# Performance work log

Hardware: AMD Instinct MI355X
Metric: run time of the kernel (lower is better)

## Reference

```python
import jax, jax.numpy as jnp
import numpy as np

D_MODEL = 1024
N_HEADS = 16
POINT_DIM = 4
PLUCKER_DIM = 6
PAIRS4 = [(0, 1), (0, 2), (0, 3), (1, 2), (1, 3), (2, 3)]
_J6 = jnp.array([[0, 0, 0, 0, 0, 1], [0, 0, 0, 0, -1, 0], [0, 0, 0, 1, 0, 0],
                 [0, 0, 1, 0, 0, 0], [0, -1, 0, 0, 0, 0], [1, 0, 0, 0, 0, 0]], dtype=jnp.float32)


def exterior(p1, p2):
    # p1, p2: [..., point_dim] -> normalized Plucker coords [..., 6]
    L = jnp.stack([p1[..., i] * p2[..., j] - p1[..., j] * p2[..., i] for i, j in PAIRS4], axis=-1)
    n = jnp.linalg.norm(L, axis=-1, keepdims=True)
    return L / jnp.maximum(n, 1e-12)


def setup_inputs() -> dict:
    key = jax.random.key(0)
    ks = jax.random.split(key, 16)
    B, T, D, H, pd = 2, 1024, D_MODEL, N_HEADS, POINT_DIM
    s = 0.02
    return {
        "x": jax.random.normal(ks[0], (B, T, D), dtype=jnp.float32),
        "qkv_w": jax.random.normal(ks[1], (D, 3 * D), dtype=jnp.float32) * s,
        "qkv_b": jnp.zeros((3 * D,), dtype=jnp.float32),
        "w1_write_w": jax.random.normal(ks[2], (2 * D, pd * H), dtype=jnp.float32) * s,
        "w2_write_w": jax.random.normal(ks[3], (D, pd * H), dtype=jnp.float32) * s,
        "w1_read_w": jax.random.normal(ks[4], (D, pd * H), dtype=jnp.float32) * s,
        "w2_read_w": jax.random.normal(ks[5], (D, pd * H), dtype=jnp.float32) * s,
        "mem_value_w": jax.random.normal(ks[6], (D, D), dtype=jnp.float32) * s,
        "mem_value_b": jnp.zeros((D,), dtype=jnp.float32),
        "mem_gate_w": jax.random.normal(ks[7], (D, H), dtype=jnp.float32) * s,
        "mem_gate_b": jnp.zeros((H,), dtype=jnp.float32),
        "mem_scale": jnp.full((H,), 0.1, dtype=jnp.float32),
        "out_w": jax.random.normal(ks[8], (D, D), dtype=jnp.float32) * s,
        "out_b": jnp.zeros((D,), dtype=jnp.float32),
        "decay_logits": jnp.full((H,), 4.6, dtype=jnp.float32),
        "J": _J6,
    }


def reference(x, qkv_w, qkv_b, w1_write_w, w2_write_w, w1_read_w, w2_read_w,
              mem_value_w, mem_value_b, mem_gate_w, mem_gate_b, mem_scale,
              out_w, out_b, decay_logits, J):
    B, T, D = x.shape
    H = N_HEADS
    dh = D // H
    pd = POINT_DIM
    scale = dh ** (-0.5)

    # ---- standard causal attention ----
    qkv = (x @ qkv_w + qkv_b).reshape(B, T, 3, H, dh)
    q = jnp.transpose(qkv[:, :, 0], (0, 2, 1, 3))  # [B,H,T,dh]
    k = jnp.transpose(qkv[:, :, 1], (0, 2, 1, 3))
    v = jnp.transpose(qkv[:, :, 2], (0, 2, 1, 3))
    scores = jnp.einsum('bhtd,bhsd->bhts', q, k) * scale
    causal_mask = jnp.triu(jnp.ones((T, T), dtype=bool), k=1)
    scores = jnp.where(causal_mask, -jnp.inf, scores)
    attn = jax.nn.softmax(scores, axis=-1)
    seq_out = jnp.einsum('bhts,bhsd->bthd', attn, v).reshape(B, T, D)

    # ---- trigram write lines ----
    z = jnp.zeros((B, 1, D), dtype=x.dtype)
    x_prev1 = jnp.concatenate([z, x[:, :-1]], axis=1)
    x_prev2 = jnp.concatenate([z, z, x[:, :-2]], axis=1)
    trigram_ctx = jnp.concatenate([x_prev2, x_prev1], axis=-1)  # [B,T,2D]
    w1 = (trigram_ctx @ w1_write_w).reshape(B, T, H, pd)
    w2 = (x @ w2_write_w).reshape(B, T, H, pd)
    write_lines = exterior(w1, w2)  # [B,T,H,6]
    r1 = (x @ w1_read_w).reshape(B, T, H, pd)
    r2 = (x @ w2_read_w).reshape(B, T, H, pd)
    read_lines = exterior(r1, r2)  # [B,T,H,6]

    # ---- Plucker incidence + decay weighting ----
    J_write = jnp.einsum('bshi,ij->bshj', write_lines, J)
    incidence = jnp.einsum('bthi,bshi->bhts', read_lines, J_write)  # [B,H,T,T]
    incidence_sq = incidence ** 2
    positions = jnp.arange(T, dtype=x.dtype)
    diffs = positions[:, None] - positions[None, :]  # [T,T]
    decays = jax.nn.sigmoid(decay_logits)  # [H]
    # strictly-causal (diffs>0) decay weights; masked_fill(triu diag=0, 0) == (diffs>0)
    weights = jnp.where(diffs[None] > 0, decays[:, None, None] ** jnp.maximum(diffs, 0.0)[None], 0.0)
    mem_score = jnp.sum(incidence_sq * weights[None], axis=-1)  # [B,H,T]

    # ---- gated memory value ----
    mem_val = x @ mem_value_w + mem_value_b  # [B,T,D]
    gate = jax.nn.sigmoid(x @ mem_gate_w + mem_gate_b)  # [B,T,H]
    mem_score_t = jnp.transpose(mem_score, (0, 2, 1))  # [B,T,H]
    gated = jax.nn.sigmoid(mem_score_t * mem_scale[None, None, :]) * gate
    gated = jnp.mean(gated, axis=-1, keepdims=True)  # [B,T,1]

    return (seq_out + gated * mem_val) @ out_w + out_b
```

## Files before the change

### kernel.cpp

```cpp
#include <hip/hip_runtime.h>
#include <hip/hip_bf16.h>
#include <stdint.h>


typedef __attribute__((ext_vector_type(8))) __bf16 bf16v8;
typedef __attribute__((ext_vector_type(8))) short  s16x8;
typedef __attribute__((ext_vector_type(4))) float  f32x4;

#define LOG2E 1.4426950408889634f

__device__ __forceinline__ float bf2f(short s) {
  union { uint32_t u; float f; } cv; cv.u = ((uint32_t)(uint16_t)s) << 16; return cv.f;
}
__device__ __forceinline__ short f2bf(float f) {
  union { float f; uint32_t u; } cv; cv.f = f;
  uint32_t r = cv.u + 0x7fffu + ((cv.u >> 16) & 1u);
  return (short)(r >> 16);
}

__device__ __forceinline__ f32x4 mfma_bf16(s16x8 a, s16x8 b, f32x4 c) {
  return __builtin_amdgcn_mfma_f32_16x16x32_bf16(
      __builtin_bit_cast(bf16v8, a), __builtin_bit_cast(bf16v8, b), c, 0, 0, 0);
}

__device__ __forceinline__ void gload_lds16(const void* g, void* l) {
  __builtin_amdgcn_global_load_lds(
      (const __attribute__((address_space(1))) uint32_t*)g,
      (__attribute__((address_space(3))) uint32_t*)l, 16, 0, 0);
}


__global__ __launch_bounds__(256) void k_prep(
    const float* __restrict__ x, const float* __restrict__ qkvw,
    const float* __restrict__ mvw, const float* __restrict__ ow,
    const float* __restrict__ w1w, const float* __restrict__ w2w,
    const float* __restrict__ r1w, const float* __restrict__ r2w,
    const float* __restrict__ gw, const float* __restrict__ qkvb,
    const float* __restrict__ mvb,
    short* __restrict__ xb, short* __restrict__ btall, short* __restrict__ owT,
    float* __restrict__ biasAll) {
  __shared__ float tile[32][33];
  const int bid = blockIdx.x;
  const int tid = threadIdx.x;
  if (bid < 2048) {
    const int i = (bid * 256 + tid) * 4;
    float4 v = *(const float4*)&x[i];
    short4 o;
    o.x = f2bf(v.x); o.y = f2bf(v.y); o.z = f2bf(v.z); o.w = f2bf(v.w);
    *(short4*)&xb[i] = o;
    return;
  }
  if (bid < 7168) {
    const float* W; short* Wt; int N, u;
    if (bid < 5120)      { W = qkvw; Wt = btall;                       N = 3072; u = bid - 2048; }
    else if (bid < 6144) { W = mvw;  Wt = btall + (size_t)3072 * 1024; N = 1024; u = bid - 5120; }
    else                 { W = ow;   Wt = owT;                         N = 1024; u = bid - 6144; }
    const int ntiles = N >> 5;
    const int n0 = (u % ntiles) * 32, k0 = (u / ntiles) * 32;
    const int tx = tid & 31, ty = tid >> 5;
#pragma unroll
    for (int i = 0; i < 4; i++)
      tile[ty + i * 8][tx] = W[(size_t)(k0 + ty + i * 8) * N + n0 + tx];
    __syncthreads();
#pragma unroll
    for (int i = 0; i < 4; i++)
      Wt[(size_t)(n0 + ty + i * 8) * 1024 + k0 + tx] = f2bf(tile[tx][ty + i * 8]);
    return;
  }
  if (bid < 8704) {
    const int idx = (bid - 7168) * 256 + tid;
    const int r = idx >> 10, k = idx & 1023;
    float v = 0.f;
    if (r < 64)       v = w1w[(size_t)k * 64 + r];
    else if (r < 128) v = w1w[(size_t)(1024 + k) * 64 + (r - 64)];
    else if (r < 192) v = w2w[(size_t)k * 64 + (r - 128)];
    else if (r < 256) v = r1w[(size_t)k * 64 + (r - 192)];
    else if (r < 320) v = r2w[(size_t)k * 64 + (r - 256)];
    else if (r < 336) v = gw[(size_t)k * 16 + (r - 320)];
    btall[(size_t)4096 * 1024 + idx] = f2bf(v);
    return;
  }
  {
    const int i = (bid - 8704) * 256 + tid;
    if (i < 4480) {
      float v = 0.f;
      if (i < 3072) v = qkvb[i];
      else if (i < 4096) v = mvb[i - 3072];
      biasAll[i] = v;
    }
  }
}


__global__ __launch_bounds__(256) void k_gemmF(const short* __restrict__ A,
                                               const short* __restrict__ Bt,
                                               short* __restrict__ C,
                                               const float* __restrict__ bias,
                                               float* __restrict__ projf,
                                               short* __restrict__ vtg) {
  const int N = 4480, K = 1024;
  __shared__ short pool[32768];
  short* Asp = pool;
  short* Bsp = pool + 16384;
  const int m0 = blockIdx.x * 128, n0 = blockIdx.y * 128;
  const int tid = threadIdx.x;
  const int lane = tid & 63, w = tid >> 6;
  const int wr = (w >> 1) * 64, wc = (w & 1) * 64;
  const int l15 = lane & 15, lg = lane >> 4;
  const int r0e = tid >> 2, c0e = (tid & 3) << 3;
  const int r1e = (tid + 256) >> 2, c1e = ((tid + 256) & 3) << 3;
  f32x4 acc[4][4] = {};

  auto stage = [&](int buf, int k0) {
    gload_lds16(A + (size_t)(m0 + r0e) * K + k0 + c0e, Asp + buf * 4096 + tid * 8);
    gload_lds16(A + (size_t)(m0 + r1e) * K + k0 + c1e, Asp + buf * 4096 + (tid + 256) * 8);
    gload_lds16(Bt + (size_t)(n0 + r0e) * K + k0 + c0e, Bsp + buf * 4096 + tid * 8);
    gload_lds16(Bt + (size_t)(n0 + r1e) * K + k0 + c1e, Bsp + buf * 4096 + (tid + 256) * 8);
  };

  stage(0, 0);
  stage(1, 32);
  __syncthreads();

  const int nkt = K >> 5;
  for (int kp = 0; kp < nkt; kp += 2) {
    if (kp + 2 < nkt) stage((kp + 2) & 3, (kp + 2) << 5);
    if (kp + 3 < nkt) stage((kp + 3) & 3, (kp + 3) << 5);
#pragma unroll
    for (int u = 0; u < 2; u++) {
      const int cur = (kp + u) & 3;
      s16x8 af[4], bfv[4];
#pragma unroll
      for (int i = 0; i < 4; i++) {
        af[i]  = *(const s16x8*)&Asp[cur * 4096 + (wr + i * 16 + l15) * 32 + lg * 8];
        bfv[i] = *(const s16x8*)&Bsp[cur * 4096 + (wc + i * 16 + l15) * 32 + lg * 8];
      }
      __builtin_amdgcn_s_setprio(1);
#pragma unroll
      for (int mi = 0; mi < 4; mi++)
#pragma unroll
        for (int ni = 0; ni < 4; ni++)
          acc[mi][ni] = mfma_bf16(af[mi], bfv[ni], acc[mi][ni]);
      __builtin_amdgcn_s_setprio(0);
    }
    __syncthreads();
  }

  const bool isproj = (n0 >= 4096);
  const bool isv = (n0 >= 2048) && (n0 < 3072);
  if (isv) {
    short* T = pool;
#pragma unroll
    for (int mi = 0; mi < 4; mi++)
#pragma unroll
      for (int ni = 0; ni < 4; ni++) {
        const int colLoc = wc + ni * 16 + l15;
        const float bv = bias[n0 + colLoc];
#pragma unroll
        for (int r = 0; r < 4; r++)
          T[colLoc * 136 + wr + mi * 16 + lg * 4 + r] = f2bf(acc[mi][ni][r] + bv);
      }
    __syncthreads();
    const int b = m0 >> 10, t0 = m0 & 1023;
#pragma unroll
    for (int q = 0; q < 8; q++) {
      const int colLoc = w * 32 + q * 4 + (lane >> 4);
      const int chunk = lane & 15;
      s16x8 v = *(const s16x8*)&T[colLoc * 136 + chunk * 8];
      const int cd = n0 + colLoc - 2048;
      const int hh = cd >> 6, d = cd & 63;
      *(s16x8*)&vtg[((size_t)((b << 4) + hh) * 64 + d) * 1024 + t0 + chunk * 8] = v;
    }
    return;
  }
#pragma unroll
  for (int mi = 0; mi < 4; mi++)
#pragma unroll
    for (int ni = 0; ni < 4; ni++) {
      const int col = n0 + wc + ni * 16 + l15;
      const float bv = bias[col];
#pragma unroll
      for (int r = 0; r < 4; r++) {
        const int row = m0 + wr + mi * 16 + lg * 4 + r;
        const float v = acc[mi][ni][r] + bv;
        if (isproj) projf[(size_t)row * 384 + (col - 4096)] = v;
        else        C[(size_t)row * 4480 + col] = f2bf(v);
      }
    }
}


template <int BM>
__global__ __launch_bounds__(256) void k_gemm(const short* __restrict__ A,
                                              const short* __restrict__ Bt,
                                              float* __restrict__ C,
                                              const float* __restrict__ bias,
                                              int N, int K) {
  constexpr int MI = BM / 32;
  __shared__ short As[4][BM * 32];
  __shared__ short Bs[4][128 * 32];
  const int m0 = blockIdx.x * BM, n0 = blockIdx.y * 128;
  const int tid = threadIdx.x;
  const int lane = tid & 63, w = tid >> 6;
  const int wr = (w >> 1) * (BM / 2), wc = (w & 1) * 64;
  const int l15 = lane & 15, lg = lane >> 4;
  const int r0e = tid >> 2, c0e = (tid & 3) << 3;
  const int r1e = (tid + 256) >> 2, c1e = ((tid + 256) & 3) << 3;
  f32x4 acc[MI][4] = {};

  auto stage = [&](int buf, int k0) {
    if constexpr (BM == 128) {
      gload_lds16(A + (size_t)(m0 + r0e) * K + k0 + c0e, &As[buf][tid * 8]);
      gload_lds16(A + (size_t)(m0 + r1e) * K + k0 + c1e, &As[buf][(tid + 256) * 8]);
    } else {
      gload_lds16(A + (size_t)(m0 + r0e) * K + k0 + c0e, &As[buf][tid * 8]);
    }
    gload_lds16(Bt + (size_t)(n0 + r0e) * K + k0 + c0e, &Bs[buf][tid * 8]);
    gload_lds16(Bt + (size_t)(n0 + r1e) * K + k0 + c1e, &Bs[buf][(tid + 256) * 8]);
  };

  stage(0, 0);
  stage(1, 32);
  __syncthreads();
  const int nkt = K >> 5;
  for (int kp = 0; kp < nkt; kp += 2) {
    if (kp + 2 < nkt) stage((kp + 2) & 3, (kp + 2) << 5);
    if (kp + 3 < nkt) stage((kp + 3) & 3, (kp + 3) << 5);
#pragma unroll
    for (int u = 0; u < 2; u++) {
      const int cur = (kp + u) & 3;
      s16x8 af[MI], bfv[4];
#pragma unroll
      for (int i = 0; i < MI; i++)
        af[i] = *(const s16x8*)&As[cur][(wr + i * 16 + l15) * 32 + lg * 8];
#pragma unroll
      for (int i = 0; i < 4; i++)
        bfv[i] = *(const s16x8*)&Bs[cur][(wc + i * 16 + l15) * 32 + lg * 8];
      __builtin_amdgcn_s_setprio(1);
#pragma unroll
      for (int mi = 0; mi < MI; mi++)
#pragma unroll
        for (int ni = 0; ni < 4; ni++)
          acc[mi][ni] = mfma_bf16(af[mi], bfv[ni], acc[mi][ni]);
      __builtin_amdgcn_s_setprio(0);
    }
    __syncthreads();
  }
#pragma unroll
  for (int mi = 0; mi < MI; mi++)
#pragma unroll
    for (int ni = 0; ni < 4; ni++) {
      const int col = n0 + wc + ni * 16 + l15;
      const float bv = bias ? bias[col] : 0.f;
#pragma unroll
      for (int r = 0; r < 4; r++) {
        const int row = m0 + wr + mi * 16 + lg * 4 + r;
        C[(size_t)row * N + col] = acc[mi][ni][r] + bv;
      }
    }
}


__global__ __launch_bounds__(256) void k_attn(const short* __restrict__ fused,
                                              const short* __restrict__ vtg,
                                              float* __restrict__ Of,
                                              float* __restrict__ Ml) {
  const int id = blockIdx.x;
  const int j = 15 - (id >> 6);
  const int rem = id & 63;
  const int sid = rem >> 5, bh = rem & 31;
  const int b = bh >> 4, h = bh & 15;
  const int tid = threadIdx.x, lane = tid & 63, w = tid >> 6;
  const int l15 = lane & 15, lg = lane >> 4;
  const int q0 = j * 64;
  const int nkv = j + 1;
  const int half = (nkv + 1) >> 1;
  const int lo = sid ? half : 0;
  const int hi = sid ? nkv : half;
  const int pidx = ((j * 32 + bh) << 1) | sid;

  __shared__ short Kl[64 * 72];
  __shared__ short Vt[64 * 72];
  __shared__ short Pl[4][16 * 72];
  const short* base = fused + (size_t)b * 1024 * 4480;
  const short* vbase = vtg + (size_t)bh * 64 * 1024;

  const int e0 = tid, e1 = tid + 256;
  const int r0e = e0 >> 3, c0e = (e0 & 7) << 3;
  const int r1e = e1 >> 3, c1e = (e1 & 7) << 3;

  s16x8 qf[2];
#pragma unroll
  for (int ks = 0; ks < 2; ks++)
    qf[ks] = *(const s16x8*)&base[(size_t)(q0 + w * 16 + l15) * 4480 +
                                  h * 64 + ks * 32 + lg * 8];

  f32x4 O[4] = {};
  float m_run[4], l_run[4];
#pragma unroll
  for (int r = 0; r < 4; r++) { m_run[r] = -1e30f; l_run[r] = 0.f; }

  if (lo < hi) {
    const int kv0 = lo * 64;
    s16x8 ka = *(const s16x8*)&base[(size_t)(kv0 + r0e) * 4480 + 1024 + h * 64 + c0e];
    s16x8 kb = *(const s16x8*)&base[(size_t)(kv0 + r1e) * 4480 + 1024 + h * 64 + c1e];
    s16x8 va = *(const s16x8*)&vbase[(size_t)r0e * 1024 + kv0 + c0e];
    s16x8 vb = *(const s16x8*)&vbase[(size_t)r1e * 1024 + kv0 + c1e];
    *(s16x8*)&Kl[r0e * 72 + c0e] = ka;
    *(s16x8*)&Kl[r1e * 72 + c1e] = kb;
    *(s16x8*)&Vt[r0e * 72 + c0e] = va;
    *(s16x8*)&Vt[r1e * 72 + c1e] = vb;
  }
  __syncthreads();

  for (int kt = lo; kt < hi; kt++) {
    const int kv0 = kt * 64;
    const bool pf = (kt + 1 < hi);
    s16x8 kn0, kn1, vn0, vn1;
    if (pf) {
      const int kvn = kv0 + 64;
      kn0 = *(const s16x8*)&base[(size_t)(kvn + r0e) * 4480 + 1024 + h * 64 + c0e];
      kn1 = *(const s16x8*)&base[(size_t)(kvn + r1e) * 4480 + 1024 + h * 64 + c1e];
      vn0 = *(const s16x8*)&vbase[(size_t)r0e * 1024 + kvn + c0e];
      vn1 = *(const s16x8*)&vbase[(size_t)r1e * 1024 + kvn + c1e];
    }

    f32x4 S[4] = {};
    __builtin_amdgcn_s_setprio(1);
#pragma unroll
    for (int sf = 0; sf < 4; sf++) {
      s16x8 kf0 = *(const s16x8*)&Kl[(sf * 16 + l15) * 72 + lg * 8];
      s16x8 kf1 = *(const s16x8*)&Kl[(sf * 16 + l15) * 72 + 32 + lg * 8];
      S[sf] = mfma_bf16(qf[0], kf0, S[sf]);
      S[sf] = mfma_bf16(qf[1], kf1, S[sf]);
    }
    __builtin_amdgcn_s_setprio(0);

    const bool diag = (kt == j);
    float sv[4][4];
#pragma unroll
    for (int sf = 0; sf < 4; sf++)
#pragma unroll
      for (int r = 0; r < 4; r++) {
        float vv = S[sf][r] * 0.125f;
        if (diag) {
          const int sg = kv0 + sf * 16 + l15;
          const int qg = q0 + w * 16 + lg * 4 + r;
          if (sg > qg) vv = -1e30f;
        }
        sv[sf][r] = vv;
      }
#pragma unroll
    for (int r = 0; r < 4; r++) {
      float pm = fmaxf(fmaxf(sv[0][r], sv[1][r]), fmaxf(sv[2][r], sv[3][r]));
      pm = fmaxf(pm, __shfl_xor(pm, 1, 64));
      pm = fmaxf(pm, __shfl_xor(pm, 2, 64));
      pm = fmaxf(pm, __shfl_xor(pm, 4, 64));
      pm = fmaxf(pm, __shfl_xor(pm, 8, 64));
      if (pm > m_run[r] + 8.f) {
        const float fac = exp2f((m_run[r] - pm) * LOG2E);
        m_run[r] = pm;
        l_run[r] *= fac;
#pragma unroll
        for (int nf = 0; nf < 4; nf++) O[nf][r] *= fac;
      }
      float rs = 0.f;
#pragma unroll
      for (int sf = 0; sf < 4; sf++) {
        float p = (sv[sf][r] <= -1e29f) ? 0.f : exp2f((sv[sf][r] - m_run[r]) * LOG2E);
        rs += p;
        Pl[w][(lg * 4 + r) * 72 + sf * 16 + l15] = f2bf(p);
      }
      rs += __shfl_xor(rs, 1, 64);
      rs += __shfl_xor(rs, 2, 64);
      rs += __shfl_xor(rs, 4, 64);
      rs += __shfl_xor(rs, 8, 64);
      l_run[r] += rs;
    }

    __builtin_amdgcn_s_setprio(1);
#pragma unroll
    for (int ks = 0; ks < 2; ks++) {
      s16x8 pfr = *(const s16x8*)&Pl[w][l15 * 72 + ks * 32 + lg * 8];
#pragma unroll
      for (int nf = 0; nf < 4; nf++) {
        s16x8 vf = *(const s16x8*)&Vt[(nf * 16 + l15) * 72 + ks * 32 + lg * 8];
        O[nf] = mfma_bf16(pfr, vf, O[nf]);
      }
    }
    __builtin_amdgcn_s_setprio(0);

    __syncthreads();
    if (pf) {
      *(s16x8*)&Kl[r0e * 72 + c0e] = kn0;
      *(s16x8*)&Kl[r1e * 72 + c1e] = kn1;
      *(s16x8*)&Vt[r0e * 72 + c0e] = vn0;
      *(s16x8*)&Vt[r1e * 72 + c1e] = vn1;
      __syncthreads();
    }
  }

  float* ob = Of + (size_t)pidx * 4096;
  float* mb = Ml + (size_t)pidx * 128;
#pragma unroll
  for (int r = 0; r < 4; r++) {
    const int rloc = w * 16 + lg * 4 + r;
#pragma unroll
    for (int nf = 0; nf < 4; nf++)
      ob[rloc * 64 + nf * 16 + l15] = O[nf][r];
    if (l15 == 0) {
      mb[rloc] = m_run[r];
      mb[64 + rloc] = l_run[r];
    }
  }
}


__device__ __forceinline__ void exterior6(const float p1[4], const float p2[4], float L[6]) {
  L[0] = p1[0] * p2[1] - p1[1] * p2[0];
  L[1] = p1[0] * p2[2] - p1[2] * p2[0];
  L[2] = p1[0] * p2[3] - p1[3] * p2[0];
  L[3] = p1[1] * p2[2] - p1[2] * p2[1];
  L[4] = p1[1] * p2[3] - p1[3] * p2[1];
  L[5] = p1[2] * p2[3] - p1[3] * p2[2];
  float n = sqrtf(L[0] * L[0] + L[1] * L[1] + L[2] * L[2] +
                  L[3] * L[3] + L[4] * L[4] + L[5] * L[5]);
  float inv = 1.f / fmaxf(n, 1e-12f);
#pragma unroll
  for (int j = 0; j < 6; j++) L[j] *= inv;
}


__global__ __launch_bounds__(1024) void k_mscan(const float* __restrict__ proj,
                                                const float* __restrict__ Jm,
                                                const float* __restrict__ dlog,
                                                float* __restrict__ ms) {
  const int bh = blockIdx.x;
  const int b = bh >> 4, h = bh & 15;
  const int t = threadIdx.x;
  const int lane = t & 63, wv = t >> 6;
  const int n = b * 1024 + t;
  const float d = 1.f / (1.f + expf(-dlog[h]));
  const float l2d = log2f(d);

  float p1[4], p2[4], L[6], Jw[6], rl[6];
#pragma unroll
  for (int p = 0; p < 4; p++) {
    float a  = (t >= 2) ? proj[(size_t)(n - 2) * 384 + h * 4 + p] : 0.f;
    float bb = (t >= 1) ? proj[(size_t)(n - 1) * 384 + 64 + h * 4 + p] : 0.f;
    p1[p] = a + bb;
    p2[p] = proj[(size_t)n * 384 + 128 + h * 4 + p];
  }
  exterior6(p1, p2, L);
#pragma unroll
  for (int j = 0; j < 6; j++) {
    float s = 0.f;
#pragma unroll
    for (int i = 0; i < 6; i++) s += L[i] * Jm[i * 6 + j];
    Jw[j] = s;
  }
#pragma unroll
  for (int p = 0; p < 4; p++) {
    p1[p] = proj[(size_t)n * 384 + 192 + h * 4 + p];
    p2[p] = proj[(size_t)n * 384 + 256 + h * 4 + p];
  }
  exterior6(p1, p2, rl);

  const float ws = exp2f(-(float)t * l2d);
  float c[21], loc[21];
  {
    int k = 0;
#pragma unroll
    for (int i = 0; i < 6; i++)
#pragma unroll
      for (int j = i; j < 6; j++) {
        loc[k] = ws * Jw[i] * Jw[j];
        c[k] = loc[k];
        k++;
      }
  }
#pragma unroll
  for (int off = 1; off < 64; off <<= 1) {
#pragma unroll
    for (int k = 0; k < 21; k++) {
      float u = __shfl_up(c[k], off, 64);
      if (lane >= off) c[k] += u;
    }
  }
  __shared__ float wsum[16][21];
  __shared__ float woff[16][21];
  if (lane == 63)
#pragma unroll
    for (int k = 0; k < 21; k++) wsum[wv][k] = c[k];
  __syncthreads();
  if (t < 21) {
    float run = 0.f;
    for (int w2 = 0; w2 < 16; w2++) { woff[w2][t] = run; run += wsum[w2][t]; }
  }
  __syncthreads();
  float q = 0.f;
  {
    int k = 0;
#pragma unroll
    for (int i = 0; i < 6; i++)
#pragma unroll
      for (int j = i; j < 6; j++) {
        const float P = woff[wv][k] + (c[k] - loc[k]);
        q += (i == j ? 1.f : 2.f) * rl[i] * rl[j] * P;
        k++;
      }
  }
  ms[(size_t)n * 16 + h] = exp2f((float)t * l2d) * q;
}


__global__ __launch_bounds__(256) void k_combine(const float* __restrict__ Of,
                                                 const float* __restrict__ Ml,
                                                 const short* __restrict__ fused,
                                                 const float* __restrict__ proj,
                                                 const float* __restrict__ ms,
                                                 const float* __restrict__ mem_scale,
                                                 const float* __restrict__ gate_b,
                                                 short* __restrict__ comb) {
  const int n = blockIdx.x;
  const int tid = threadIdx.x;
  __shared__ float gsh;
  if (tid < 16) {
    const float gp = proj[(size_t)n * 384 + 320 + tid] + gate_b[tid];
    const float g = 1.f / (1.f + expf(-gp));
    const float sc = ms[(size_t)n * 16 + tid] * mem_scale[tid];
    const float sg = 1.f / (1.f + expf(-sc));
    float v = sg * g;
    v += __shfl_xor(v, 1, 64);
    v += __shfl_xor(v, 2, 64);
    v += __shfl_xor(v, 4, 64);
    v += __shfl_xor(v, 8, 64);
    if (tid == 0) gsh = v * (1.f / 16.f);
  }
  __syncthreads();
  const float g = gsh;
  const int b = n >> 10, t = n & 1023;
  const int c0 = tid * 4;
  const int h = c0 >> 6, coff = c0 & 63;
  const int bh = b * 16 + h;
  const int p = ((t >> 6) * 32 + bh) << 1;
  const int rloc = t & 63;
  const float m0v = Ml[(size_t)p * 128 + rloc];
  const float l0v = Ml[(size_t)p * 128 + 64 + rloc];
  const float m1v = Ml[(size_t)(p + 1) * 128 + rloc];
  const float l1v = Ml[(size_t)(p + 1) * 128 + 64 + rloc];
  const float M = fmaxf(m0v, m1v);
  const float w0 = exp2f((m0v - M) * LOG2E);
  const float w1 = exp2f((m1v - M) * LOG2E);
  const float inv = 1.f / (w0 * l0v + w1 * l1v);
  f32x4 o0 = *(const f32x4*)&Of[(size_t)p * 4096 + rloc * 64 + coff];
  f32x4 o1 = *(const f32x4*)&Of[(size_t)(p + 1) * 4096 + rloc * 64 + coff];
  short4 mvv = *(const short4*)&fused[(size_t)n * 4480 + 3072 + c0];
  short4 ov;
  ov.x = f2bf((w0 * o0[0] + w1 * o1[0]) * inv + g * bf2f(mvv.x));
  ov.y = f2bf((w0 * o0[1] + w1 * o1[1]) * inv + g * bf2f(mvv.y));
  ov.z = f2bf((w0 * o0[2] + w1 * o1[2]) * inv + g * bf2f(mvv.z));
  ov.w = f2bf((w0 * o0[3] + w1 * o1[3]) * inv + g * bf2f(mvv.w));
  *(short4*)&comb[(size_t)n * 1024 + c0] = ov;
}


extern "C" void kernel_launch(void* const* d_in, const int* in_sizes, int n_in,
                              void* d_out, int out_size, void* d_ws, size_t ws_size,
                              hipStream_t stream) {
  const float* x    = (const float*)d_in[0];
  const float* qkvw = (const float*)d_in[1];
  const float* qkvb = (const float*)d_in[2];
  const float* w1w  = (const float*)d_in[3];
  const float* w2w  = (const float*)d_in[4];
  const float* r1w  = (const float*)d_in[5];
  const float* r2w  = (const float*)d_in[6];
  const float* mvw  = (const float*)d_in[7];
  const float* mvb  = (const float*)d_in[8];
  const float* gw   = (const float*)d_in[9];
  const float* gb   = (const float*)d_in[10];
  const float* msc  = (const float*)d_in[11];
  const float* ow   = (const float*)d_in[12];
  const float* ob   = (const float*)d_in[13];
  const float* dlog = (const float*)d_in[14];
  const float* Jm   = (const float*)d_in[15];
  float* out = (float*)d_out;

  char* wsp = (char*)d_ws;
  auto alloc = [&](size_t bytes) {
    char* p = wsp;
    wsp += (bytes + 255) & ~(size_t)255;
    return p;
  };
  short* xb     = (short*)alloc((size_t)2048 * 1024 * 2);
  short* btall  = (short*)alloc((size_t)4480 * 1024 * 2);
  short* owT    = (short*)alloc((size_t)1024 * 1024 * 2);
  short* fusedC = (short*)alloc((size_t)2048 * 4480 * 2);
  float* projf  = (float*)alloc((size_t)2048 * 384 * 4);
  float* biasA  = (float*)alloc((size_t)4480 * 4);
  short* vtg    = (short*)alloc((size_t)32 * 64 * 1024 * 2);
  short* comb   = (short*)alloc((size_t)2048 * 1024 * 2);
  float* msb    = (float*)alloc((size_t)2048 * 16 * 4);
  float* Of     = (float*)alloc((size_t)1024 * 4096 * 4);
  float* Mlb    = (float*)alloc((size_t)1024 * 128 * 4);

  k_prep<<<8722, 256, 0, stream>>>(x, qkvw, mvw, ow, w1w, w2w, r1w, r2w, gw,
                                   qkvb, mvb, xb, btall, owT, biasA);

  k_gemmF<<<dim3(16, 35), 256, 0, stream>>>(xb, btall, fusedC, biasA, projf, vtg);

  k_attn<<<1024, 256, 0, stream>>>(fusedC, vtg, Of, Mlb);

  k_mscan<<<32, 1024, 0, stream>>>(projf, Jm, dlog, msb);
  k_combine<<<2048, 256, 0, stream>>>(Of, Mlb, fusedC, projf, msb, msc, gb, comb);

  k_gemm<64><<<dim3(32, 8), 256, 0, stream>>>(comb, owT, out, ob, 1024, 1024);
}
```

Before: 116.4 us.

## Fold memory-score scan into attention kernel as extra blocks

Removes the separate k_mscan launch and runs its work as 32 extra blocks appended to the k_attn grid. Each of these blocks uses 256 threads, each handling 4 timesteps, and scans the 21 quadratic terms one at a time with shuffles and shared-memory syncs instead of holding all 21 in registers. The aim is to drop one kernel launch and let the small scan overlap with attention blocks. The per-term loop adds many __syncthreads calls, and sharing one kernel may change register pressure or occupancy for the attention path.

```diff
diff --git a/kernel.cpp b/kernel.cpp
--- a/kernel.cpp
+++ b/kernel.cpp
@@ -261,16 +261,119 @@
 }
 
 
+__device__ __forceinline__ void exterior6(const float p1[4], const float p2[4], float L[6]) {
+  L[0] = p1[0] * p2[1] - p1[1] * p2[0];
+  L[1] = p1[0] * p2[2] - p1[2] * p2[0];
+  L[2] = p1[0] * p2[3] - p1[3] * p2[0];
+  L[3] = p1[1] * p2[2] - p1[2] * p2[1];
+  L[4] = p1[1] * p2[3] - p1[3] * p2[1];
+  L[5] = p1[2] * p2[3] - p1[3] * p2[2];
+  float n = sqrtf(L[0] * L[0] + L[1] * L[1] + L[2] * L[2] +
+                  L[3] * L[3] + L[4] * L[4] + L[5] * L[5]);
+  float inv = 1.f / fmaxf(n, 1e-12f);
+#pragma unroll
+  for (int j = 0; j < 6; j++) L[j] *= inv;
+}
+
+
 __global__ __launch_bounds__(256) void k_attn(const short* __restrict__ fused,
                                               const short* __restrict__ vtg,
                                               float* __restrict__ Of,
-                                              float* __restrict__ Ml) {
+                                              float* __restrict__ Ml,
+                                              const float* __restrict__ proj,
+                                              const float* __restrict__ Jm,
+                                              const float* __restrict__ dlog,
+                                              float* __restrict__ ms) {
   const int id = blockIdx.x;
+  const int tid = threadIdx.x;
+
+  __shared__ short Kl[64 * 72];
+  __shared__ short Vt[64 * 72];
+  __shared__ short Pl[4][16 * 72];
+  __shared__ float wsumS[4];
+
+  if (id >= 1024) {
+    const int bh2 = id - 1024;
+    const int b2 = bh2 >> 4, h2 = bh2 & 15;
+    const int lane2 = tid & 63, wv2 = tid >> 6;
+    const int t0 = tid * 4;
+    const float d = 1.f / (1.f + expf(-dlog[h2]));
+    const float l2d = log2f(d);
+
+    float Jw[4][6], rr[4][6], wsv[4], iwsv[4];
+#pragma unroll
+    for (int u = 0; u < 4; u++) {
+      const int t = t0 + u;
+      const int n = b2 * 1024 + t;
+      float p1[4], p2[4], L[6];
+#pragma unroll
+      for (int p = 0; p < 4; p++) {
+        float a  = (t >= 2) ? proj[(size_t)(n - 2) * 384 + h2 * 4 + p] : 0.f;
+        float bb = (t >= 1) ? proj[(size_t)(n - 1) * 384 + 64 + h2 * 4 + p] : 0.f;
+        p1[p] = a + bb;
+        p2[p] = proj[(size_t)n * 384 + 128 + h2 * 4 + p];
+      }
+      exterior6(p1, p2, L);
+#pragma unroll
+      for (int j = 0; j < 6; j++) {
+        float s = 0.f;
+#pragma unroll
+        for (int i = 0; i < 6; i++) s += L[i] * Jm[i * 6 + j];
+        Jw[u][j] = s;
+      }
+#pragma unroll
+      for (int p = 0; p < 4; p++) {
+        p1[p] = proj[(size_t)n * 384 + 192 + h2 * 4 + p];
+        p2[p] = proj[(size_t)n * 384 + 256 + h2 * 4 + p];
+      }
+      exterior6(p1, p2, L);
+#pragma unroll
+      for (int j = 0; j < 6; j++) rr[u][j] = L[j];
+      wsv[u]  = exp2f(-(float)t * l2d);
+      iwsv[u] = exp2f((float)t * l2d);
+    }
+
+    float q[4] = {0.f, 0.f, 0.f, 0.f};
+#pragma unroll
+    for (int i = 0; i < 6; i++)
+#pragma unroll
+      for (int j = i; j < 6; j++) {
+        const float v0 = wsv[0] * Jw[0][i] * Jw[0][j];
+        const float v1 = wsv[1] * Jw[1][i] * Jw[1][j];
+        const float v2 = wsv[2] * Jw[2][i] * Jw[2][j];
+        const float v3 = wsv[3] * Jw[3][i] * Jw[3][j];
+        const float s1 = v0 + v1, s2 = s1 + v2, s3 = s2 + v3;
+        float c = s3;
+#pragma unroll
+        for (int off = 1; off < 64; off <<= 1) {
+          float uu = __shfl_up(c, off, 64);
+          if (lane2 >= off) c += uu;
+        }
+        if (lane2 == 63) wsumS[wv2] = c;
+        __syncthreads();
+        float base = 0.f;
+#pragma unroll
+        for (int w2 = 0; w2 < 4; w2++)
+          if (w2 < wv2) base += wsumS[w2];
+        __syncthreads();
+        const float et = base + (c - s3);
+        const float coef = (i == j) ? 1.f : 2.f;
+        q[0] += coef * rr[0][i] * rr[0][j] * et;
+        q[1] += coef * rr[1][i] * rr[1][j] * (et + v0);
+        q[2] += coef * rr[2][i] * rr[2][j] * (et + s1);
+        q[3] += coef * rr[3][i] * rr[3][j] * (et + s2);
+      }
+#pragma unroll
+    for (int u = 0; u < 4; u++)
+      ms[((size_t)(b2 * 1024 + t0 + u)) * 16 + h2] = iwsv[u] * q[u];
+    return;
+  }
+
   const int j = 15 - (id >> 6);
   const int rem = id & 63;
   const int sid = rem >> 5, bh = rem & 31;
   const int b = bh >> 4, h = bh & 15;
-  const int tid = threadIdx.x, lane = tid & 63, w = tid >> 6;
+  const int lane = tid & 63, w = tid >> 6;
   const int l15 = lane & 15, lg = lane >> 4;
   const int q0 = j * 64;
   const int nkv = j + 1;
@@ -279,9 +382,6 @@
   const int hi = sid ? nkv : half;
   const int pidx = ((j * 32 + bh) << 1) | sid;
 
-  __shared__ short Kl[64 * 72];
-  __shared__ short Vt[64 * 72];
-  __shared__ short Pl[4][16 * 72];
   const short* base = fused + (size_t)b * 1024 * 4480;
   const short* vbase = vtg + (size_t)bh * 64 * 1024;
 
@@ -413,104 +513,6 @@
       mb[64 + rloc] = l_run[r];
     }
   }
-}
-
-
-__device__ __forceinline__ void exterior6(const float p1[4], const float p2[4], float L[6]) {
-  L[0] = p1[0] * p2[1] - p1[1] * p2[0];
-  L[1] = p1[0] * p2[2] - p1[2] * p2[0];
-  L[2] = p1[0] * p2[3] - p1[3] * p2[0];
-  L[3] = p1[1] * p2[2] - p1[2] * p2[1];
-  L[4] = p1[1] * p2[3] - p1[3] * p2[1];
-  L[5] = p1[2] * p2[3] - p1[3] * p2[2];
-  float n = sqrtf(L[0] * L[0] + L[1] * L[1] + L[2] * L[2] +
-                  L[3] * L[3] + L[4] * L[4] + L[5] * L[5]);
-  float inv = 1.f / fmaxf(n, 1e-12f);
-#pragma unroll
-  for (int j = 0; j < 6; j++) L[j] *= inv;
-}
-
-
-__global__ __launch_bounds__(1024) void k_mscan(const float* __restrict__ proj,
-                                                const float* __restrict__ Jm,
-                                                const float* __restrict__ dlog,
-                                                float* __restrict__ ms) {
-  const int bh = blockIdx.x;
-  const int b = bh >> 4, h = bh & 15;
-  const int t = threadIdx.x;
-  const int lane = t & 63, wv = t >> 6;
-  const int n = b * 1024 + t;
-  const float d = 1.f / (1.f + expf(-dlog[h]));
-  const float l2d = log2f(d);
-
-  float p1[4], p2[4], L[6], Jw[6], rl[6];
-#pragma unroll
-  for (int p = 0; p < 4; p++) {
-    float a  = (t >= 2) ? proj[(size_t)(n - 2) * 384 + h * 4 + p] : 0.f;
-    float bb = (t >= 1) ? proj[(size_t)(n - 1) * 384 + 64 + h * 4 + p] : 0.f;
-    p1[p] = a + bb;
-    p2[p] = proj[(size_t)n * 384 + 128 + h * 4 + p];
-  }
-  exterior6(p1, p2, L);
-#pragma unroll
-  for (int j = 0; j < 6; j++) {
-    float s = 0.f;
-#pragma unroll
-    for (int i = 0; i < 6; i++) s += L[i] * Jm[i * 6 + j];
-    Jw[j] = s;
-  }
-#pragma unroll
-  for (int p = 0; p < 4; p++) {
-    p1[p] = proj[(size_t)n * 384 + 192 + h * 4 + p];
-    p2[p] = proj[(size_t)n * 384 + 256 + h * 4 + p];
-  }
-  exterior6(p1, p2, rl);
-
-  const float ws = exp2f(-(float)t * l2d);
-  float c[21], loc[21];
-  {
-    int k = 0;
-#pragma unroll
-    for (int i = 0; i < 6; i++)
-#pragma unroll
-      for (int j = i; j < 6; j++) {
-        loc[k] = ws * Jw[i] * Jw[j];
-        c[k] = loc[k];
-        k++;
-      }
-  }
-#pragma unroll
-  for (int off = 1; off < 64; off <<= 1) {
-#pragma unroll
-    for (int k = 0; k < 21; k++) {
-      float u = __shfl_up(c[k], off, 64);
-      if (lane >= off) c[k] += u;
-    }
-  }
-  __shared__ float wsum[16][21];
-  __shared__ float woff[16][21];
-  if (lane == 63)
-#pragma unroll
-    for (int k = 0; k < 21; k++) wsum[wv][k] = c[k];
-  __syncthreads();
-  if (t < 21) {
-    float run = 0.f;
-    for (int w2 = 0; w2 < 16; w2++) { woff[w2][t] = run; run += wsum[w2][t]; }
-  }
-  __syncthreads();
-  float q = 0.f;
-  {
-    int k = 0;
-#pragma unroll
-    for (int i = 0; i < 6; i++)
-#pragma unroll
-      for (int j = i; j < 6; j++) {
-        const float P = woff[wv][k] + (c[k] - loc[k]);
-        q += (i == j ? 1.f : 2.f) * rl[i] * rl[j] * P;
-        k++;
-      }
-  }
-  ms[(size_t)n * 16 + h] = exp2f((float)t * l2d) * q;
 }
 
 
@@ -609,9 +611,8 @@
 
   k_gemmF<<<dim3(16, 35), 256, 0, stream>>>(xb, btall, fusedC, biasA, projf, vtg);
 
-  k_attn<<<1024, 256, 0, stream>>>(fusedC, vtg, Of, Mlb);
-
-  k_mscan<<<32, 1024, 0, stream>>>(projf, Jm, dlog, msb);
+  k_attn<<<1056, 256, 0, stream>>>(fusedC, vtg, Of, Mlb, projf, Jm, dlog, msb);
+
   k_combine<<<2048, 256, 0, stream>>>(Of, Mlb, fusedC, projf, msb, msc, gb, comb);
 
   k_gemm<64><<<dim3(32, 8), 256, 0, stream>>>(comb, owT, out, ob, 1024, 1024);
```

Result: slower. 131.8 us (+13.2%).
